# Kernel tuning notes

Measured on AMD Instinct MI355X. Metric: run time of the kernel, lower is better.

## Reference

```python
import jax, jax.numpy as jnp
import numpy as np

H = 384
W = 384
C_X = 64       # channels of x (== out_channels)
C_PTX = 64     # channels of ptx
C_IN = C_X + C_PTX  # Linear in_channels = 128
C_OUT = 64
N_TGT = 120000  # number of target pixels (CSR segments)
DEG = 8         # points per target pixel
N_PTS = N_TGT * DEG


def setup_inputs() -> dict:
    key = jax.random.key(0)
    k1, k2, k3, k4 = jax.random.split(key, 4)
    x = jax.random.normal(k1, (1, C_X, H, W), jnp.float32)
    ptx = jax.random.normal(k2, (N_PTS, C_PTX), jnp.float32)
    # CSR row pointer over points per target pixel (monotone, ends at N_PTS)
    point_key = jnp.arange(N_TGT + 1, dtype=jnp.int32) * DEG
    # unique target-pixel indices into H*W
    pixel_tgt_idx = jnp.arange(N_TGT, dtype=jnp.int32)
    sm_w = jax.random.normal(k3, (C_IN, 1), jnp.float32) * 0.05
    sm_b = jnp.zeros((1,), jnp.float32)
    fo_w = jax.random.normal(k4, (C_IN, C_OUT), jnp.float32) * 0.05
    fo_b = jnp.zeros((C_OUT,), jnp.float32)
    return {"x": x, "ptx": ptx, "sm_w": sm_w, "sm_b": sm_b,
            "fo_w": fo_w, "fo_b": fo_b, "point_key": point_key,
            "pixel_tgt_idx": pixel_tgt_idx, "bs": 1, "height": H, "width": W}


def reference(x, ptx, sm_w, sm_b, fo_w, fo_b, point_key, pixel_tgt_idx, bs, height, width):
    # segment id per point from CSR rowptr (static total length for jit)
    seg = jnp.repeat(jnp.arange(N_TGT, dtype=jnp.int32), jnp.diff(point_key),
                     total_repeat_length=N_PTS)
    # pixel features gathered to target pixels, then CSR-gathered to points
    feat_px = x.transpose(0, 2, 3, 1).reshape(height * width, C_X)[pixel_tgt_idx]
    feat = jnp.concatenate([ptx, feat_px[seg]], axis=1)  # [N_PTS, C_IN]
    # _net_forward: identity (base class)
    # segment softmax over points within each pixel group
    logits = feat @ sm_w + sm_b  # [N_PTS, 1]
    m = jax.ops.segment_max(logits, seg, num_segments=N_TGT)
    e = jnp.exp(logits - m[seg])
    s = jax.ops.segment_sum(e, seg, num_segments=N_TGT)
    weight = e / (s[seg] + 1e-16)
    # feat_out projection replaces ptx
    ptx_out = feat @ fo_w + fo_b  # [N_PTS, C_OUT]
    agg = jax.ops.segment_sum(weight * ptx_out, seg, num_segments=N_TGT)  # [N_TGT, C_OUT]
    # list_to_map: scatter aggregated features back to image grid + mask
    flat = jnp.zeros((height * width, C_OUT), x.dtype).at[pixel_tgt_idx].set(agg)
    mask = jnp.zeros((height * width, 1), x.dtype).at[pixel_tgt_idx].set(1.0)
    fmap = flat.reshape(1, height, width, C_OUT).transpose(0, 3, 1, 2)
    mmap = mask.reshape(1, height, width, 1).transpose(0, 3, 1, 2)
    x_out = jnp.where(mmap > 0, fmap, x)
    return x_out, ptx_out
```

## Files before the change

### kernel.cpp

```cpp
#include <hip/hip_runtime.h>
#include <hip/hip_bf16.h>
#include <math.h>

typedef __attribute__((ext_vector_type(8))) short short8v;
typedef __attribute__((ext_vector_type(4))) float float4v;

#define TB 64

__device__ __forceinline__ short f2bf(float f) {
    __hip_bfloat16 h = __float2bfloat16(f);
    short s; __builtin_memcpy(&s, &h, sizeof(short));
    return s;
}
__device__ __forceinline__ float4v mfma_bf16(short8v a, short8v b, float4v c) {
    return __builtin_amdgcn_mfma_f32_16x16x32_bf16(a, b, c, 0, 0, 0);
}

__global__ __launch_bounds__(256)
void copy_x_kernel(const float4* __restrict__ x, float4* __restrict__ out, int n4) {
    int i = blockIdx.x * blockDim.x + threadIdx.x;
    if (i < n4) out[i] = x[i];
}

__global__ __launch_bounds__(256, 4)
void fused_kernel(const float* __restrict__ x,
                  const float* __restrict__ ptx,
                  const float* __restrict__ sm_w,
                  const float* __restrict__ fo_w,
                  const float* __restrict__ fo_b,
                  const int* __restrict__ point_key,
                  const int* __restrict__ pixel_tgt_idx,
                  float* __restrict__ xout,
                  float* __restrict__ ptx_out,
                  int n_tgt, int n_pts, int hw)
{
    __shared__ __align__(16) char sraw[34816];
    unsigned short (*fpx)[72] = (unsigned short (*)[72])sraw;
    unsigned short (*wT)[72]  = (unsigned short (*)[72])(sraw + 9216);
    float (*q_lds)[68]        = (float (*)[68])sraw;
    float (*agg)[68]          = (float (*)[68])(sraw + 17408);
    __shared__ int pix_s[TB], r0_s[TB], deg_s[TB];

    const int tid  = threadIdx.x;
    const int lane = tid & 63;
    const int w    = tid >> 6;
    const int lo16 = lane & 15;
    const int g    = lane >> 4;
    const int t0   = blockIdx.x * TB;
    const int tw0  = w * 16;

    float4 wv[8];
    {
        const float4* fw4 = (const float4*)fo_w;
        #pragma unroll
        for (int i = 0; i < 8; ++i) wv[i] = fw4[i * 256 + tid];
    }
    if (tid < TB) {
        int t = t0 + tid;
        bool v = t < n_tgt;
        int r0 = v ? point_key[t] : 0;
        int d  = v ? (point_key[t + 1] - r0) : 0;
        pix_s[tid] = v ? pixel_tgt_idx[t] : 0;
        r0_s[tid]  = r0;
        deg_s[tid] = d > 8 ? 8 : d;
    }
    float fb[4];
    #pragma unroll
    for (int ct = 0; ct < 4; ++ct) fb[ct] = fo_b[ct * 16 + lo16];

    #pragma unroll
    for (int i = 0; i < 8; ++i) {
        int flat = (i * 256 + tid) * 4;
        int k = flat >> 6, c = flat & 63;
        int wrow0 = (k & 64) + c;
        int col = k & 63;
        wT[wrow0 + 0][col] = (unsigned short)f2bf(wv[i].x);
        wT[wrow0 + 1][col] = (unsigned short)f2bf(wv[i].y);
        wT[wrow0 + 2][col] = (unsigned short)f2bf(wv[i].z);
        wT[wrow0 + 3][col] = (unsigned short)f2bf(wv[i].w);
    }
    __syncthreads();

    {
        const int tgt = tid >> 2, q4 = tid & 3;
        const int pix = pix_s[tgt];
        const float* xp = x + (size_t)(q4 * 16) * hw + pix;
        #pragma unroll
        for (int hhalf = 0; hhalf < 2; ++hhalf) {
            short8v pk;
            #pragma unroll
            for (int j = 0; j < 8; ++j)
                pk[j] = f2bf(xp[(size_t)(hhalf * 8 + j) * hw]);
            *(short8v*)&fpx[tgt][q4 * 16 + hhalf * 8] = pk;
        }
    }

    short8v b1[5][2];
    #pragma unroll
    for (int ct = 0; ct < 4; ++ct)
        #pragma unroll
        for (int kh = 0; kh < 2; ++kh)
            b1[ct][kh] = *(const short8v*)&wT[ct * 16 + lo16][kh * 32 + g * 8];
    #pragma unroll
    for (int kh = 0; kh < 2; ++kh) {
        short8v bb;
        #pragma unroll
        for (int j = 0; j < 8; ++j)
            bb[j] = (lo16 == 0) ? f2bf(sm_w[kh * 32 + g * 8 + j]) : (short)0;
        b1[4][kh] = bb;
    }
    __syncthreads();

    float4v qv4[4];
    {
        short8v a20 = *(const short8v*)&fpx[tw0 + lo16][g * 8];
        short8v a21 = *(const short8v*)&fpx[tw0 + lo16][32 + g * 8];
        #pragma unroll
        for (int ct = 0; ct < 4; ++ct) {
            short8v b20 = *(const short8v*)&wT[64 + ct * 16 + lo16][g * 8];
            short8v b21 = *(const short8v*)&wT[64 + ct * 16 + lo16][32 + g * 8];
            float4v z = {0.f, 0.f, 0.f, 0.f};
            z = mfma_bf16(a20, b20, z);
            qv4[ct] = mfma_bf16(a21, b21, z);
        }
    }
    __syncthreads();
    #pragma unroll
    for (int ct = 0; ct < 4; ++ct)
        #pragma unroll
        for (int r = 0; r < 4; ++r)
            q_lds[tw0 + g * 4 + r][ct * 16 + lo16] = qv4[ct][r] + fb[ct];

    float4 buf0, buf1, buf2, buf3;
    auto LOADA = [&](int mt) {
        const int tlA = tw0 + mt * 2 + (lo16 >> 3);
        int pg = r0_s[tlA] + (lo16 & 7);
        if (pg >= n_pts) pg = n_pts - 1;
        const float* prow = ptx + (size_t)pg * 64 + g * 8;
        buf0 = *(const float4*)(prow);
        buf1 = *(const float4*)(prow + 4);
        buf2 = *(const float4*)(prow + 32);
        buf3 = *(const float4*)(prow + 36);
    };
    LOADA(0);
    #pragma unroll
    for (int mt = 0; mt < 8; ++mt) {
        const float4 c0 = buf0, c1 = buf1, c2 = buf2, c3 = buf3;
        if (mt < 7) LOADA(mt + 1);

        short8v a0, a1;
        a0[0] = f2bf(c0.x); a0[1] = f2bf(c0.y); a0[2] = f2bf(c0.z); a0[3] = f2bf(c0.w);
        a0[4] = f2bf(c1.x); a0[5] = f2bf(c1.y); a0[6] = f2bf(c1.z); a0[7] = f2bf(c1.w);
        a1[0] = f2bf(c2.x); a1[1] = f2bf(c2.y); a1[2] = f2bf(c2.z); a1[3] = f2bf(c2.w);
        a1[4] = f2bf(c3.x); a1[5] = f2bf(c3.y); a1[6] = f2bf(c3.z); a1[7] = f2bf(c3.w);

        float4v c[5];
        #pragma unroll
        for (int ct = 0; ct < 5; ++ct) {
            float4v z = {0.f, 0.f, 0.f, 0.f};
            z = mfma_bf16(a0, b1[ct][0], z);
            c[ct] = mfma_bf16(a1, b1[ct][1], z);
        }

        const int tE   = tw0 + mt * 2 + (g >> 1);
        const int degE = deg_s[tE];
        const int r0E  = r0_s[tE];
        float lgt[4];
        #pragma unroll
        for (int r = 0; r < 4; ++r) {
            float v = __shfl(c[4][r], lane & 48);
            lgt[r] = (((g & 1) * 4 + r) < degE) ? v : -3.4e38f;
        }
        float m4 = fmaxf(fmaxf(lgt[0], lgt[1]), fmaxf(lgt[2], lgt[3]));
        float m8 = fmaxf(m4, __shfl_xor(m4, 16));
        float wgt[4], wsum = 0.f;
        #pragma unroll
        for (int r = 0; r < 4; ++r) {
            int pE = (g & 1) * 4 + r;
            wgt[r] = (pE < degE) ? __expf(lgt[r] - m8) : 0.0f;
            wsum += wgt[r];
        }
        wsum += __shfl_xor(wsum, 16);
        const float inv = 1.0f / (wsum + 1e-16f);

        #pragma unroll
        for (int ct = 0; ct < 4; ++ct) {
            const int col = ct * 16 + lo16;
            const float qv = q_lds[tE][col];
            float ap = 0.f;
            #pragma unroll
            for (int r = 0; r < 4; ++r) {
                float po = c[ct][r] + qv;
                int pE = (g & 1) * 4 + r;
                if (pE < degE)
                    ptx_out[(size_t)(r0E + pE) * 64 + col] = po;
                ap = fmaf(wgt[r] * inv, po, ap);
            }
            ap += __shfl_xor(ap, 16);
            if (!(lane & 16)) agg[tE][col] = ap;
        }
    }
    __syncthreads();

    {
        const int tgt = tid >> 2, q4 = tid & 3;
        if (t0 + tgt < n_tgt) {
            const int pix = pix_s[tgt];
            float* xp = xout + (size_t)(q4 * 16) * hw + pix;
            #pragma unroll
            for (int u = 0; u < 4; ++u) {
                float4 v = *(const float4*)&agg[tgt][q4 * 16 + u * 4];
                xp[(size_t)(u * 4 + 0) * hw] = v.x;
                xp[(size_t)(u * 4 + 1) * hw] = v.y;
                xp[(size_t)(u * 4 + 2) * hw] = v.z;
                xp[(size_t)(u * 4 + 3) * hw] = v.w;
            }
        }
    }
}

extern "C" void kernel_launch(void* const* d_in, const int* in_sizes, int n_in,
                              void* d_out, int out_size, void* d_ws, size_t ws_size,
                              hipStream_t stream) {
    const float* x             = (const float*)d_in[0];
    const float* ptx           = (const float*)d_in[1];
    const float* sm_w          = (const float*)d_in[2];
    const float* fo_w          = (const float*)d_in[4];
    const float* fo_b          = (const float*)d_in[5];
    const int*   point_key     = (const int*)d_in[6];
    const int*   pixel_tgt_idx = (const int*)d_in[7];

    const int x_elems = in_sizes[0];
    const int hw      = x_elems / 64;
    const int n_tgt   = in_sizes[7];
    const int n_pts   = in_sizes[1] / 64;

    float* xout    = (float*)d_out;
    float* ptx_out = xout + (size_t)x_elems;

    const int n4 = x_elems / 4;
    copy_x_kernel<<<(n4 + 255) / 256, 256, 0, stream>>>(
        (const float4*)x, (float4*)xout, n4);

    const int blocks = (n_tgt + TB - 1) / TB;
    fused_kernel<<<blocks, 256, 0, stream>>>(
        x, ptx, sm_w, fo_w, fo_b, point_key, pixel_tgt_idx,
        xout, ptx_out, n_tgt, n_pts, hw);
}
```

Measured before the change: 143.0 us.

## Software-pipeline MFMA and epilogue, swizzle weight LDS, precompute gather indices

Restructures the main loop so the MFMA for tile mt overlaps with the softmax/store epilogue of tile mt-1, using double-buffered accumulators. The first ptx load is issued earlier, before the x-projection MFMAs. Gather row indices are precomputed into registers. The transposed weight tile in LDS gets an XOR swizzle to cut bank conflicts. The logit column is replicated across all lanes by filling the sm_w operand everywhere, which removes a shuffle. The cost is higher register pressure from the extra accumulators and index array.

```diff
diff --git a/kernel.cpp b/kernel.cpp
--- a/kernel.cpp
+++ b/kernel.cpp
@@ -14,6 +14,10 @@
 }
 __device__ __forceinline__ float4v mfma_bf16(short8v a, short8v b, float4v c) {
     return __builtin_amdgcn_mfma_f32_16x16x32_bf16(a, b, c, 0, 0, 0);
+}
+
+__device__ __forceinline__ int WTI(int row, int col) {
+    return row * 72 + (col ^ ((((row) >> 2) & 7) << 3));
 }
 
 __global__ __launch_bounds__(256)
@@ -36,7 +40,7 @@
 {
     __shared__ __align__(16) char sraw[34816];
     unsigned short (*fpx)[72] = (unsigned short (*)[72])sraw;
-    unsigned short (*wT)[72]  = (unsigned short (*)[72])(sraw + 9216);
+    unsigned short* wTf       = (unsigned short*)(sraw + 9216);
     float (*q_lds)[68]        = (float (*)[68])sraw;
     float (*agg)[68]          = (float (*)[68])(sraw + 17408);
     __shared__ int pix_s[TB], r0_s[TB], deg_s[TB];
@@ -74,12 +78,20 @@
         int k = flat >> 6, c = flat & 63;
         int wrow0 = (k & 64) + c;
         int col = k & 63;
-        wT[wrow0 + 0][col] = (unsigned short)f2bf(wv[i].x);
-        wT[wrow0 + 1][col] = (unsigned short)f2bf(wv[i].y);
-        wT[wrow0 + 2][col] = (unsigned short)f2bf(wv[i].z);
-        wT[wrow0 + 3][col] = (unsigned short)f2bf(wv[i].w);
-    }
-    __syncthreads();
+        wTf[WTI(wrow0 + 0, col)] = (unsigned short)f2bf(wv[i].x);
+        wTf[WTI(wrow0 + 1, col)] = (unsigned short)f2bf(wv[i].y);
+        wTf[WTI(wrow0 + 2, col)] = (unsigned short)f2bf(wv[i].z);
+        wTf[WTI(wrow0 + 3, col)] = (unsigned short)f2bf(wv[i].w);
+    }
+    __syncthreads();
+
+    int pgm[8];
+    #pragma unroll
+    for (int mt = 0; mt < 8; ++mt) {
+        int tlA = tw0 + mt * 2 + (lo16 >> 3);
+        int pg  = r0_s[tlA] + (lo16 & 7);
+        pgm[mt] = pg < n_pts ? pg : n_pts - 1;
+    }
 
     {
         const int tgt = tid >> 2, q4 = tid & 3;
@@ -100,14 +112,23 @@
     for (int ct = 0; ct < 4; ++ct)
         #pragma unroll
         for (int kh = 0; kh < 2; ++kh)
-            b1[ct][kh] = *(const short8v*)&wT[ct * 16 + lo16][kh * 32 + g * 8];
+            b1[ct][kh] = *(const short8v*)&wTf[WTI(ct * 16 + lo16, kh * 32 + g * 8)];
     #pragma unroll
     for (int kh = 0; kh < 2; ++kh) {
         short8v bb;
         #pragma unroll
         for (int j = 0; j < 8; ++j)
-            bb[j] = (lo16 == 0) ? f2bf(sm_w[kh * 32 + g * 8 + j]) : (short)0;
+            bb[j] = f2bf(sm_w[kh * 32 + g * 8 + j]);
         b1[4][kh] = bb;
+    }
+
+    float4 lb0, lb1, lb2, lb3;
+    {
+        const float* prow = ptx + (size_t)pgm[0] * 64 + g * 8;
+        lb0 = *(const float4*)(prow);
+        lb1 = *(const float4*)(prow + 4);
+        lb2 = *(const float4*)(prow + 32);
+        lb3 = *(const float4*)(prow + 36);
     }
     __syncthreads();
 
@@ -117,8 +138,8 @@
         short8v a21 = *(const short8v*)&fpx[tw0 + lo16][32 + g * 8];
         #pragma unroll
         for (int ct = 0; ct < 4; ++ct) {
-            short8v b20 = *(const short8v*)&wT[64 + ct * 16 + lo16][g * 8];
-            short8v b21 = *(const short8v*)&wT[64 + ct * 16 + lo16][32 + g * 8];
+            short8v b20 = *(const short8v*)&wTf[WTI(64 + ct * 16 + lo16, g * 8)];
+            short8v b21 = *(const short8v*)&wTf[WTI(64 + ct * 16 + lo16, 32 + g * 8)];
             float4v z = {0.f, 0.f, 0.f, 0.f};
             z = mfma_bf16(a20, b20, z);
             qv4[ct] = mfma_bf16(a21, b21, z);
@@ -131,46 +152,16 @@
         for (int r = 0; r < 4; ++r)
             q_lds[tw0 + g * 4 + r][ct * 16 + lo16] = qv4[ct][r] + fb[ct];
 
-    float4 buf0, buf1, buf2, buf3;
-    auto LOADA = [&](int mt) {
-        const int tlA = tw0 + mt * 2 + (lo16 >> 3);
-        int pg = r0_s[tlA] + (lo16 & 7);
-        if (pg >= n_pts) pg = n_pts - 1;
-        const float* prow = ptx + (size_t)pg * 64 + g * 8;
-        buf0 = *(const float4*)(prow);
-        buf1 = *(const float4*)(prow + 4);
-        buf2 = *(const float4*)(prow + 32);
-        buf3 = *(const float4*)(prow + 36);
-    };
-    LOADA(0);
-    #pragma unroll
-    for (int mt = 0; mt < 8; ++mt) {
-        const float4 c0 = buf0, c1 = buf1, c2 = buf2, c3 = buf3;
-        if (mt < 7) LOADA(mt + 1);
-
-        short8v a0, a1;
-        a0[0] = f2bf(c0.x); a0[1] = f2bf(c0.y); a0[2] = f2bf(c0.z); a0[3] = f2bf(c0.w);
-        a0[4] = f2bf(c1.x); a0[5] = f2bf(c1.y); a0[6] = f2bf(c1.z); a0[7] = f2bf(c1.w);
-        a1[0] = f2bf(c2.x); a1[1] = f2bf(c2.y); a1[2] = f2bf(c2.z); a1[3] = f2bf(c2.w);
-        a1[4] = f2bf(c3.x); a1[5] = f2bf(c3.y); a1[6] = f2bf(c3.z); a1[7] = f2bf(c3.w);
-
-        float4v c[5];
-        #pragma unroll
-        for (int ct = 0; ct < 5; ++ct) {
-            float4v z = {0.f, 0.f, 0.f, 0.f};
-            z = mfma_bf16(a0, b1[ct][0], z);
-            c[ct] = mfma_bf16(a1, b1[ct][1], z);
-        }
-
+    float4v cfr[2][5];
+
+    auto EPIL = [&](int mt, const float4v* c) {
         const int tE   = tw0 + mt * 2 + (g >> 1);
         const int degE = deg_s[tE];
         const int r0E  = r0_s[tE];
         float lgt[4];
         #pragma unroll
-        for (int r = 0; r < 4; ++r) {
-            float v = __shfl(c[4][r], lane & 48);
-            lgt[r] = (((g & 1) * 4 + r) < degE) ? v : -3.4e38f;
-        }
+        for (int r = 0; r < 4; ++r)
+            lgt[r] = (((g & 1) * 4 + r) < degE) ? c[4][r] : -3.4e38f;
         float m4 = fmaxf(fmaxf(lgt[0], lgt[1]), fmaxf(lgt[2], lgt[3]));
         float m8 = fmaxf(m4, __shfl_xor(m4, 16));
         float wgt[4], wsum = 0.f;
@@ -182,7 +173,6 @@
         }
         wsum += __shfl_xor(wsum, 16);
         const float inv = 1.0f / (wsum + 1e-16f);
-
         #pragma unroll
         for (int ct = 0; ct < 4; ++ct) {
             const int col = ct * 16 + lo16;
@@ -199,7 +189,34 @@
             ap += __shfl_xor(ap, 16);
             if (!(lane & 16)) agg[tE][col] = ap;
         }
-    }
+    };
+
+    #pragma unroll
+    for (int mt = 0; mt < 8; ++mt) {
+        short8v a0, a1;
+        a0[0] = f2bf(lb0.x); a0[1] = f2bf(lb0.y); a0[2] = f2bf(lb0.z); a0[3] = f2bf(lb0.w);
+        a0[4] = f2bf(lb1.x); a0[5] = f2bf(lb1.y); a0[6] = f2bf(lb1.z); a0[7] = f2bf(lb1.w);
+        a1[0] = f2bf(lb2.x); a1[1] = f2bf(lb2.y); a1[2] = f2bf(lb2.z); a1[3] = f2bf(lb2.w);
+        a1[4] = f2bf(lb3.x); a1[5] = f2bf(lb3.y); a1[6] = f2bf(lb3.z); a1[7] = f2bf(lb3.w);
+
+        if (mt < 7) {
+            const float* prow = ptx + (size_t)pgm[mt + 1] * 64 + g * 8;
+            lb0 = *(const float4*)(prow);
+            lb1 = *(const float4*)(prow + 4);
+            lb2 = *(const float4*)(prow + 32);
+            lb3 = *(const float4*)(prow + 36);
+        }
+
+        #pragma unroll
+        for (int ct = 0; ct < 5; ++ct) {
+            float4v z = {0.f, 0.f, 0.f, 0.f};
+            z = mfma_bf16(a0, b1[ct][0], z);
+            cfr[mt & 1][ct] = mfma_bf16(a1, b1[ct][1], z);
+        }
+
+        if (mt > 0) EPIL(mt - 1, cfr[(mt - 1) & 1]);
+    }
+    EPIL(7, cfr[1]);
     __syncthreads();
 
     {
```

Measured after the change: 180.8 us. 1.26x slower.
